# Kernel optimization log

Hardware: AMD Instinct MI355X
Metric: run time of the kernel (lower is better)

The kernel has to match this reference:

```python
import jax, jax.numpy as jnp
import numpy as np

WIN = 7
N = WIN * WIN  # 49 tokens per window
C = 384
H = 12
HD = C // H
B_ = 4096
NW = 64  # number of distinct window masks; must divide B_


def _relative_position_index(wh=WIN, ww=WIN):
    coords = np.stack(np.meshgrid(np.arange(wh), np.arange(ww), indexing='ij'))  # [2,wh,ww]
    cf = coords.reshape(2, -1)
    rel = cf[:, :, None] - cf[:, None, :]               # [2,N,N]
    rel = rel.transpose(1, 2, 0).astype(np.int32)       # [N,N,2]
    rel[:, :, 0] += wh - 1
    rel[:, :, 1] += ww - 1
    rel[:, :, 0] *= 2 * ww - 1
    return jnp.asarray(rel.sum(-1))                     # [N,N] int32


def setup_inputs() -> dict:
    key = jax.random.key(0)
    ks = jax.random.split(key, 8)
    std = 0.02
    return {
        'x': jax.random.normal(ks[0], (B_, N, C), jnp.float32),
        'mask': jnp.zeros((NW, N, N), jnp.float32),  # 0/-inf mask; zeros here
        'qkv_w': jax.random.normal(ks[1], (3 * C, C), jnp.float32) * std,
        'qkv_b': jnp.zeros((3 * C,), jnp.float32),
        'rpb_table': jax.random.normal(ks[2], ((2 * WIN - 1) ** 2, H), jnp.float32) * std,
        'proj_l_w': jax.random.normal(ks[3], (H, H), jnp.float32) * std,
        'proj_l_b': jnp.zeros((H,), jnp.float32),
        'proj_w_w': jax.random.normal(ks[4], (H, H), jnp.float32) * std,
        'proj_w_b': jnp.zeros((H,), jnp.float32),
        'proj_weight': jax.random.normal(ks[5], (C, C), jnp.float32) * std,
        'proj_bias': jnp.zeros((C,), jnp.float32),
        'rel_index': _relative_position_index(),
    }


def reference(x, mask, qkv_w, qkv_b, rpb_table, proj_l_w, proj_l_b,
              proj_w_w, proj_w_b, proj_weight, proj_bias, rel_index):
    B, n, c = x.shape
    scale = HD ** (-0.5)
    qkv = x @ qkv_w.T + qkv_b                     # [B,N,3C]
    q_out, k_out, v_out = jnp.split(qkv, 3, axis=-1)  # each [B,N,C]
    qkv5 = qkv.reshape(B, n, 3, H, HD)
    q = qkv5[:, :, 0].transpose(0, 2, 1, 3)       # [B,H,N,hd]
    k = qkv5[:, :, 1].transpose(0, 2, 1, 3)
    v = qkv5[:, :, 2].transpose(0, 2, 1, 3)
    attn = jnp.einsum('bhnd,bhmd->bhnm', q * scale, k)   # [B,H,N,N]
    bias = rpb_table[rel_index]                   # [N,N,H]
    attn = attn + bias.transpose(2, 0, 1)[None]
    # proj_l: linear mixing across heads (Linear acts on last dim after permute)
    attn = jnp.einsum('bhnm,gh->bgnm', attn, proj_l_w) + proj_l_b[None, :, None, None]
    nW = mask.shape[0]
    attn = attn.reshape(B // nW, nW, H, n, n) + mask[None, :, None]
    attn = attn.reshape(B, H, n, n)
    attn = jax.nn.softmax(attn, axis=-1)
    # proj_w: head mixing after softmax
    attn = jnp.einsum('bhnm,gh->bgnm', attn, proj_w_w) + proj_w_b[None, :, None, None]
    out = jnp.einsum('bhnm,bhmd->bnhd', attn, v).reshape(B, n, c)
    out = out @ proj_weight.T + proj_bias
    return (out, (q_out, k_out, v_out))
```

## Files before the change

### kernel.cpp

```cpp
#include <hip/hip_runtime.h>
#include <hip/hip_bf16.h>

#define TOK 49
#define NPT 2401
#define CDIM 384
#define NH 12
#define HDIM 32
#define NWIN 64
#define BTOT 4096
#define OUTSZ (BTOT * TOK * CDIM)
#define L2E 1.4426950408889634f

typedef __attribute__((ext_vector_type(8))) short bf16x8;
typedef __attribute__((ext_vector_type(4))) float f32x4;
typedef unsigned int uint32;
typedef unsigned short ushort_t;

__device__ inline ushort_t f2bf(float f) {
  uint32 u = __float_as_uint(f);
  u += 0x7FFF + ((u >> 16) & 1);
  return (ushort_t)(u >> 16);
}
__device__ inline uint32 pk2(float a, float b) {
  union { __hip_bfloat162 h; uint32 u; } x;
  x.h = __float22bfloat162_rn(float2{a, b});
  return x.u;
}
__device__ inline float bf2f(uint32 u) { return __uint_as_float((u & 0xffffu) << 16); }
__device__ inline bf16x8 pack8(float4 a, float4 b) {
  union { __hip_bfloat162 h[4]; bf16x8 v; } u;
  u.h[0] = __float22bfloat162_rn(float2{a.x, a.y});
  u.h[1] = __float22bfloat162_rn(float2{a.z, a.w});
  u.h[2] = __float22bfloat162_rn(float2{b.x, b.y});
  u.h[3] = __float22bfloat162_rn(float2{b.z, b.w});
  return u.v;
}
__device__ inline bf16x8 pack8f(const float* f) {
  union { __hip_bfloat162 h[4]; bf16x8 v; } u;
#pragma unroll
  for (int i = 0; i < 4; ++i) u.h[i] = __float22bfloat162_rn(float2{f[2*i], f[2*i+1]});
  return u.v;
}

__global__ void k_cvt(const float* __restrict__ src, ushort_t* __restrict__ dst, int n8) {
  int i = blockIdx.x * 256 + threadIdx.x;
  if (i >= n8) return;
  const float4* s = (const float4*)(src + (size_t)i * 8);
  float4 a = s[0], b = s[1];
  uint4 o;
  o.x = (uint32)f2bf(a.x) | ((uint32)f2bf(a.y) << 16);
  o.y = (uint32)f2bf(a.z) | ((uint32)f2bf(a.w) << 16);
  o.z = (uint32)f2bf(b.x) | ((uint32)f2bf(b.y) << 16);
  o.w = (uint32)f2bf(b.z) | ((uint32)f2bf(b.w) << 16);
  *(uint4*)(dst + (size_t)i * 8) = o;
}

__global__ void k_bias(const float* __restrict__ rpb, const float* __restrict__ plw,
                       const float* __restrict__ plb, float* __restrict__ bm) {
  int i = blockIdx.x * 256 + threadIdx.x;
  if (i >= 169 * 16) return;
  int rid = i >> 4, g = i & 15;
  float s = 0.f;
  if (g < NH) {
    s = plb[g];
#pragma unroll
    for (int h = 0; h < NH; ++h) s = fmaf(plw[g * NH + h], rpb[rid * NH + h], s);
    s *= L2E;
  }
  bm[i] = s;
}

__launch_bounds__(256)
__global__ void k_qkv_mfma(const ushort_t* __restrict__ Xb, const ushort_t* __restrict__ Wb,
                           const float* __restrict__ Bq, float* __restrict__ qslab) {
  __shared__ ushort_t As[128 * 32];
  __shared__ ushort_t Bs[128 * 32];
  const int bid = blockIdx.x;
  const int sw = (bid & 7) * 1764 + (bid >> 3);
  const int bx = sw / 9;
  const int by = sw - bx * 9;
  const int tid = threadIdx.x;
  const int l = tid & 63;
  const int wv = tid >> 6;
  const int wr = wv >> 1, wc = wv & 1;
  const int row0 = bx * 128;
  const int col0 = by * 128;

  f32x4 acc[4][4];
#pragma unroll
  for (int i = 0; i < 4; ++i)
#pragma unroll
    for (int j = 0; j < 4; ++j)
#pragma unroll
      for (int e = 0; e < 4; ++e) acc[i][j][e] = 0.f;

  for (int kb = 0; kb < CDIM; kb += 32) {
#pragma unroll
    for (int i = 0; i < 2; ++i) {
      int cid = tid + i * 256;
      int r = cid >> 2, c = cid & 3;
      uint4 v = *(const uint4*)&Xb[(size_t)(row0 + r) * CDIM + kb + c * 8];
      *(uint4*)&As[r * 32 + c * 8] = v;
      uint4 w = *(const uint4*)&Wb[(size_t)(col0 + r) * CDIM + kb + c * 8];
      *(uint4*)&Bs[r * 32 + c * 8] = w;
    }
    __syncthreads();
    bf16x8 af[4], bfr[4];
#pragma unroll
    for (int mt = 0; mt < 4; ++mt)
      af[mt] = *(const bf16x8*)&As[(wr * 64 + mt * 16 + (l & 15)) * 32 + (l >> 4) * 8];
#pragma unroll
    for (int nt = 0; nt < 4; ++nt)
      bfr[nt] = *(const bf16x8*)&Bs[(wc * 64 + nt * 16 + (l & 15)) * 32 + (l >> 4) * 8];
#pragma unroll
    for (int mt = 0; mt < 4; ++mt)
#pragma unroll
      for (int nt = 0; nt < 4; ++nt)
        acc[mt][nt] = __builtin_amdgcn_mfma_f32_16x16x32_bf16(af[mt], bfr[nt], acc[mt][nt], 0, 0, 0);
    __syncthreads();
  }

  const int slab = by / 3;
  const int cslab0 = col0 - slab * CDIM;
  float* dst = qslab + (size_t)slab * OUTSZ;
#pragma unroll
  for (int nt = 0; nt < 4; ++nt) {
    int colg = col0 + wc * 64 + nt * 16 + (l & 15);
    int colo = cslab0 + wc * 64 + nt * 16 + (l & 15);
    float bv = Bq[colg];
#pragma unroll
    for (int mt = 0; mt < 4; ++mt) {
      int rbase = row0 + wr * 64 + mt * 16 + (l >> 4) * 4;
#pragma unroll
      for (int j = 0; j < 4; ++j)
        dst[(size_t)(rbase + j) * CDIM + colo] = acc[mt][nt][j] + bv;
    }
  }
}

__launch_bounds__(1024, 8)
__global__ void k_attn9(const float* __restrict__ qslab, const float* __restrict__ kslab,
                        const float* __restrict__ vslab, const float* __restrict__ mask,
                        const float* __restrict__ bmg, const int* __restrict__ relidx,
                        const float* __restrict__ plw, const float* __restrict__ pww,
                        const float* __restrict__ pwb, float* __restrict__ xout) {
  __shared__ __align__(16) ushort_t SA[19976];
  __shared__ __align__(16) ushort_t PP[12 * 1400 + 416];
  __shared__ __align__(16) ushort_t bm16[169 * 12 + 4];
  __shared__ ushort_t ridx_s[1240];

  const int tid = threadIdx.x;
  const int b  = blockIdx.x >> 1;
  const int bh = blockIdx.x & 1;
  const int n0 = bh * 25;
  const int NR = bh ? 24 : 25;
  const size_t base = (size_t)b * TOK * CDIM;
  const int l = tid & 63, l15 = l & 15, l16 = l >> 4;
  const int wv = tid >> 6;
  const float SCL = 0.17677669529663687f * L2E;

  for (int i = tid; i < 169 * 12; i += 1024) {
    int rid = i / 12, g = i - rid * 12;
    bm16[i] = f2bf(bmg[rid * 16 + g]);
  }
  for (int i = tid; i < 1240; i += 1024) {
    int pg = i + n0 * 49; if (pg > 2400) pg = 2400;
    ridx_s[i] = (ushort_t)relidx[pg];
  }
  for (int p = tid; p < 1240; p += 1024) *(uint2*)&SA[p * 16 + 12] = uint2{0u, 0u};
  if (tid < 580) *(uint32*)&SA[18816 + tid * 2] = 0u;
  if (tid < 208) *(uint32*)&PP[12 * 1400 + tid * 2] = 0u;

  {
    const int art = wv >> 3;
    const int act = (wv >> 1) & 3;
    const int ah0 = (wv & 1) * 6;
    const int nrow = art * 16 + l15;
    const int mrow = act * 16 + l15;
    const bool qv = nrow < NR;
    const bool kv = mrow < TOK;
#pragma unroll
    for (int hp = 0; hp < 3; ++hp) {
      f32x4 s2[2];
#pragma unroll
      for (int hh = 0; hh < 2; ++hh) {
        int h = ah0 + hp * 2 + hh;
        bf16x8 af = {0,0,0,0,0,0,0,0}, bf = {0,0,0,0,0,0,0,0};
        if (qv) {
          const float4* qp = (const float4*)(qslab + base + (size_t)(n0 + nrow) * CDIM + h * HDIM + l16 * 8);
          af = pack8(qp[0], qp[1]);
        }
        if (kv) {
          const float4* kp = (const float4*)(kslab + base + (size_t)mrow * CDIM + h * HDIM + l16 * 8);
          bf = pack8(kp[0], kp[1]);
        }
        f32x4 z = {0.f, 0.f, 0.f, 0.f};
        s2[hh] = __builtin_amdgcn_mfma_f32_16x16x32_bf16(af, bf, z, 0, 0, 0);
      }
#pragma unroll
      for (int j = 0; j < 4; ++j) {
        int nj = art * 16 + l16 * 4 + j;
        if (nj < NR && kv)
          *(uint32*)&SA[(nj * 49 + mrow) * 16 + ah0 + hp * 2] = pk2(s2[0][j], s2[1][j]);
      }
    }
  }
  __syncthreads();

  {
    const float* maskw = mask + (size_t)(b & (NWIN - 1)) * NPT;
    float apf[8], bpf[8];
#pragma unroll
    for (int j = 0; j < 8; ++j) {
      int kj = l16 * 8 + j;
      apf[j] = (l15 < NH && kj < NH) ? plw[l15 * NH + kj] * SCL : 0.f;
      bpf[j] = (l15 < NH && kj < NH) ? pww[l15 * NH + kj] : 0.f;
    }
    const bf16x8 aplw = pack8f(apf);
    const bf16x8 bpww = pack8f(bpf);
    const float pwbv = (l15 < NH) ? pwb[l15] : 0.f;

    for (int nl = wv; nl < NR; nl += 16) {
      const int pb0 = nl * 49;
      float ev[4][4];
      float rs[4] = {0.f, 0.f, 0.f, 0.f};
#pragma unroll
      for (int mc = 0; mc < 4; ++mc) {
        int m = mc * 16 + l15;
        int pl = pb0 + m;
        bf16x8 sf = {0,0,0,0,0,0,0,0};
        if (l16 < 2) sf = *(const bf16x8*)&SA[pl * 16 + l16 * 8];
        int rid = (int)ridx_s[pl];
        uint2 bmu = *(const uint2*)&bm16[rid * 12 + l16 * 4];
        int pg = pl + n0 * 49; if (pg > 2400) pg = 2400;
        float mk = maskw[pg] * L2E;
        f32x4 cini = {bf2f(bmu.x) + mk, bf2f(bmu.x >> 16) + mk,
                      bf2f(bmu.y) + mk, bf2f(bmu.y >> 16) + mk};
        f32x4 o = __builtin_amdgcn_mfma_f32_16x16x32_bf16(aplw, sf, cini, 0, 0, 0);
        bool okm = (m < TOK);
#pragma unroll
        for (int j = 0; j < 4; ++j) {
          int g = l16 * 4 + j;
          float e = (okm && g < NH) ? exp2f(o[j]) : 0.f;
          ev[mc][j] = e;
          rs[j] += e;
        }
      }
#pragma unroll
      for (int d = 1; d < 16; d <<= 1)
#pragma unroll
        for (int j = 0; j < 4; ++j) rs[j] += __shfl_xor(rs[j], d, 64);
      float inv[4];
#pragma unroll
      for (int j = 0; j < 4; ++j) inv[j] = (rs[j] > 0.f) ? 1.f / rs[j] : 0.f;

#pragma unroll
      for (int mc = 0; mc < 4; ++mc) {
        int m = mc * 16 + l15;
        if (m < TOK) {
          uint2 w;
          w.x = pk2(ev[mc][0] * inv[0], ev[mc][1] * inv[1]);
          w.y = pk2(ev[mc][2] * inv[2], ev[mc][3] * inv[3]);
          *(uint2*)&SA[(pb0 + m) * 16 + l16 * 4] = w;
        }
      }
#pragma unroll
      for (int mc = 0; mc < 4; ++mc) {
        bf16x8 pf8 = {0,0,0,0,0,0,0,0};
        if (l16 < 2) pf8 = *(const bf16x8*)&SA[(pb0 + mc * 16 + l15) * 16 + l16 * 8];
        f32x4 cd = {pwbv, pwbv, pwbv, pwbv};
        f32x4 o = __builtin_amdgcn_mfma_f32_16x16x32_bf16(pf8, bpww, cd, 0, 0, 0);
        int m0 = mc * 16 + l16 * 4;
        if (l15 < NH && m0 < 56) {
          float z0 = (m0     < TOK) ? o[0] : 0.f;
          float z1 = (m0 + 1 < TOK) ? o[1] : 0.f;
          float z2 = (m0 + 2 < TOK) ? o[2] : 0.f;
          float z3 = (m0 + 3 < TOK) ? o[3] : 0.f;
          uint2 w;
          w.x = pk2(z0, z1);
          w.y = pk2(z2, z3);
          *(uint2*)&PP[l15 * 1400 + nl * 56 + m0] = w;
        }
      }
    }
  }
  __syncthreads();

  {
    ushort_t* Vt = SA;
    for (int i = tid; i < CDIM * 13; i += 1024) {
      int mq = i / CDIM, c = i - mq * CDIM;
      int m = mq * 4;
      float f0 = (m     < TOK) ? vslab[base + (size_t)(m    ) * CDIM + c] : 0.f;
      float f1 = (m + 1 < TOK) ? vslab[base + (size_t)(m + 1) * CDIM + c] : 0.f;
      float f2 = (m + 2 < TOK) ? vslab[base + (size_t)(m + 2) * CDIM + c] : 0.f;
      float f3 = (m + 3 < TOK) ? vslab[base + (size_t)(m + 3) * CDIM + c] : 0.f;
      uint2 u;
      u.x = pk2(f0, f1);
      u.y = pk2(f2, f3);
      *(uint2*)&Vt[c * 52 + mq * 4] = u;
    }
  }
  __syncthreads();

  {
    const ushort_t* Vt = SA;
    const int ert = wv >> 3;
    const int edt = (wv >> 2) & 1;
    const int egq = wv & 3;
#pragma unroll
    for (int gi = 0; gi < 3; ++gi) {
      int g = egq * 3 + gi;
      int col = g * HDIM + edt * 16 + l15;
      f32x4 acc = {0.f, 0.f, 0.f, 0.f};
#pragma unroll
      for (int ks = 0; ks < 2; ++ks) {
        bf16x8 pa8 = {0,0,0,0,0,0,0,0};
        bf16x8 vb8 = {0,0,0,0,0,0,0,0};
        if (!(ks == 1 && l16 == 3)) {
          pa8 = *(const bf16x8*)&PP[g * 1400 + (ert * 16 + l15) * 56 + ks * 32 + l16 * 8];
          uint2 lo = *(const uint2*)&Vt[col * 52 + ks * 32 + l16 * 8];
          uint2 hi = *(const uint2*)&Vt[col * 52 + ks * 32 + l16 * 8 + 4];
          union { uint32 u[4]; bf16x8 v; } uv;
          uv.u[0] = lo.x; uv.u[1] = lo.y; uv.u[2] = hi.x; uv.u[3] = hi.y;
          vb8 = uv.v;
        }
        acc = __builtin_amdgcn_mfma_f32_16x16x32_bf16(pa8, vb8, acc, 0, 0, 0);
      }
#pragma unroll
      for (int j = 0; j < 4; ++j) {
        int nlo = ert * 16 + l16 * 4 + j;
        if (nlo < NR)
          xout[base + (size_t)(n0 + nlo) * CDIM + col] = acc[j];
      }
    }
  }
}

__launch_bounds__(512, 4)
__global__ void k_proj3(float* __restrict__ Y, const float* __restrict__ W,
                        const float* __restrict__ Bv) {
  __shared__ __align__(16) ushort_t Asb[64 * 392];
  __shared__ __align__(16) ushort_t Bsb[384 * 40];
  const int tid = threadIdx.x;
  const int l = tid & 63, l15 = l & 15, l16 = l >> 4;
  const int wv = tid >> 6;
  const int wr = wv >> 2;
  const int wc = wv & 3;
  const int row0 = blockIdx.x * 64;

#pragma unroll
  for (int i = 0; i < 6; ++i) {
    int cid = tid + i * 512;
    int r = cid / 48, c8 = cid - (cid / 48) * 48;
    const float4* s = (const float4*)&Y[(size_t)(row0 + r) * CDIM + c8 * 8];
    float4 a = s[0], b = s[1];
    uint4 o;
    o.x = pk2(a.x, a.y); o.y = pk2(a.z, a.w);
    o.z = pk2(b.x, b.y); o.w = pk2(b.z, b.w);
    *(uint4*)&Asb[r * 392 + c8 * 8] = o;
  }

  f32x4 acc[2][6];
#pragma unroll
  for (int i = 0; i < 2; ++i)
#pragma unroll
    for (int j = 0; j < 6; ++j)
#pragma unroll
      for (int e = 0; e < 4; ++e) acc[i][j][e] = 0.f;

  for (int kb = 0; kb < 12; ++kb) {
    __syncthreads();
#pragma unroll
    for (int i = 0; i < 3; ++i) {
      int cid = tid + i * 512;
      int col = cid >> 2, k8 = cid & 3;
      const float4* s = (const float4*)&W[(size_t)col * CDIM + kb * 32 + k8 * 8];
      float4 a = s[0], b = s[1];
      uint4 o;
      o.x = pk2(a.x, a.y); o.y = pk2(a.z, a.w);
      o.z = pk2(b.x, b.y); o.w = pk2(b.z, b.w);
      *(uint4*)&Bsb[col * 40 + k8 * 8] = o;
    }
    __syncthreads();
    bf16x8 af[2], bfr[6];
#pragma unroll
    for (int mt = 0; mt < 2; ++mt)
      af[mt] = *(const bf16x8*)&Asb[(wr * 32 + mt * 16 + l15) * 392 + kb * 32 + l16 * 8];
#pragma unroll
    for (int nt = 0; nt < 6; ++nt)
      bfr[nt] = *(const bf16x8*)&Bsb[(wc * 96 + nt * 16 + l15) * 40 + l16 * 8];
#pragma unroll
    for (int mt = 0; mt < 2; ++mt)
#pragma unroll
      for (int nt = 0; nt < 6; ++nt)
        acc[mt][nt] = __builtin_amdgcn_mfma_f32_16x16x32_bf16(af[mt], bfr[nt], acc[mt][nt], 0, 0, 0);
  }

#pragma unroll
  for (int nt = 0; nt < 6; ++nt) {
    int col = wc * 96 + nt * 16 + l15;
    float bv = Bv[col];
#pragma unroll
    for (int mt = 0; mt < 2; ++mt) {
      int rbase = row0 + wr * 32 + mt * 16 + l16 * 4;
#pragma unroll
      for (int j = 0; j < 4; ++j)
        Y[(size_t)(rbase + j) * CDIM + col] = acc[mt][nt][j] + bv;
    }
  }
}

extern "C" void kernel_launch(void* const* d_in, const int* in_sizes, int n_in,
                              void* d_out, int out_size, void* d_ws, size_t ws_size,
                              hipStream_t stream) {
  const float* x      = (const float*)d_in[0];
  const float* mask   = (const float*)d_in[1];
  const float* qkv_w  = (const float*)d_in[2];
  const float* qkv_b  = (const float*)d_in[3];
  const float* rpb    = (const float*)d_in[4];
  const float* plw    = (const float*)d_in[5];
  const float* plb    = (const float*)d_in[6];
  const float* pww    = (const float*)d_in[7];
  const float* pwb    = (const float*)d_in[8];
  const float* projw  = (const float*)d_in[9];
  const float* projb  = (const float*)d_in[10];
  const int*   relidx = (const int*)d_in[11];

  float* out   = (float*)d_out;
  float* qslab = out + (size_t)OUTSZ;
  float* kslab = out + 2 * (size_t)OUTSZ;
  float* vslab = out + 3 * (size_t)OUTSZ;

  ushort_t* Xb = (ushort_t*)out;
  ushort_t* Wb = (ushort_t*)(out + 70000000);
  float*    bm = (float*)d_ws;

  k_cvt<<<(OUTSZ / 8 + 255) / 256, 256, 0, stream>>>(x, Xb, OUTSZ / 8);
  k_cvt<<<(3 * CDIM * CDIM / 8 + 255) / 256, 256, 0, stream>>>(qkv_w, Wb, 3 * CDIM * CDIM / 8);
  k_bias<<<(169 * 16 + 255) / 256, 256, 0, stream>>>(rpb, plw, plb, bm);

  k_qkv_mfma<<<(BTOT * TOK / 128) * 9, 256, 0, stream>>>(Xb, Wb, qkv_b, qslab);

  k_attn9<<<BTOT * 2, 1024, 0, stream>>>(qslab, kslab, vslab, mask, bm, relidx,
                                         plw, pww, pwb, out);

  k_proj3<<<BTOT * TOK / 64, 512, 0, stream>>>(out, projw, projb);
}
```

Before: 1.350 ms.

## Fuse output projection into attention kernel via LDS-staged bf16 attention output

The output projection GEMM now runs at the end of the attention kernel, which previously ran as a separate kernel. Each block stages its per-window attention output as bf16 in shared memory. Its 16 waves then multiply that tile against a pre-converted bf16 projection weight read from global memory, adding the bias before the store. This removes the fp32 round trip of the attention output through HBM and one kernel launch. In exchange, every block re-reads the 384x384 weight from L2/global with no LDS reuse, the MFMA work is uneven across waves (only 8 of 16 take a second column tile), and the 25/24-row halves are padded to 32 rows.

```diff
diff --git a/kernel.cpp b/kernel.cpp
--- a/kernel.cpp
+++ b/kernel.cpp
@@ -139,11 +139,12 @@
 }
 
 __launch_bounds__(1024, 8)
-__global__ void k_attn9(const float* __restrict__ qslab, const float* __restrict__ kslab,
-                        const float* __restrict__ vslab, const float* __restrict__ mask,
-                        const float* __restrict__ bmg, const int* __restrict__ relidx,
-                        const float* __restrict__ plw, const float* __restrict__ pww,
-                        const float* __restrict__ pwb, float* __restrict__ xout) {
+__global__ void k_attn10(const float* __restrict__ qslab, const float* __restrict__ kslab,
+                         const float* __restrict__ vslab, const float* __restrict__ mask,
+                         const float* __restrict__ bmg, const int* __restrict__ relidx,
+                         const float* __restrict__ plw, const float* __restrict__ pww,
+                         const float* __restrict__ pwb, const ushort_t* __restrict__ Wb2,
+                         const float* __restrict__ pjb, float* __restrict__ xout) {
   __shared__ __align__(16) ushort_t SA[19976];
   __shared__ __align__(16) ushort_t PP[12 * 1400 + 416];
   __shared__ __align__(16) ushort_t bm16[169 * 12 + 4];
@@ -303,11 +304,12 @@
   }
   __syncthreads();
 
+  f32x4 acc3[3];
+  const int ert = wv >> 3;
+  const int edt = (wv >> 2) & 1;
+  const int egq = wv & 3;
   {
     const ushort_t* Vt = SA;
-    const int ert = wv >> 3;
-    const int edt = (wv >> 2) & 1;
-    const int egq = wv & 3;
 #pragma unroll
     for (int gi = 0; gi < 3; ++gi) {
       int g = egq * 3 + gi;
@@ -327,86 +329,78 @@
         }
         acc = __builtin_amdgcn_mfma_f32_16x16x32_bf16(pa8, vb8, acc, 0, 0, 0);
       }
+      acc3[gi] = acc;
+    }
+  }
+  __syncthreads();
+
+  {
+    ushort_t* AO = SA;
+#pragma unroll
+    for (int gi = 0; gi < 3; ++gi) {
+      int g = egq * 3 + gi;
+      int col = g * HDIM + edt * 16 + l15;
 #pragma unroll
       for (int j = 0; j < 4; ++j) {
         int nlo = ert * 16 + l16 * 4 + j;
-        if (nlo < NR)
-          xout[base + (size_t)(n0 + nlo) * CDIM + col] = acc[j];
-      }
-    }
-  }
-}
-
-__launch_bounds__(512, 4)
-__global__ void k_proj3(float* __restrict__ Y, const float* __restrict__ W,
-                        const float* __restrict__ Bv) {
-  __shared__ __align__(16) ushort_t Asb[64 * 392];
-  __shared__ __align__(16) ushort_t Bsb[384 * 40];
-  const int tid = threadIdx.x;
-  const int l = tid & 63, l15 = l & 15, l16 = l >> 4;
-  const int wv = tid >> 6;
-  const int wr = wv >> 2;
-  const int wc = wv & 3;
-  const int row0 = blockIdx.x * 64;
-
-#pragma unroll
-  for (int i = 0; i < 6; ++i) {
-    int cid = tid + i * 512;
-    int r = cid / 48, c8 = cid - (cid / 48) * 48;
-    const float4* s = (const float4*)&Y[(size_t)(row0 + r) * CDIM + c8 * 8];
-    float4 a = s[0], b = s[1];
-    uint4 o;
-    o.x = pk2(a.x, a.y); o.y = pk2(a.z, a.w);
-    o.z = pk2(b.x, b.y); o.w = pk2(b.z, b.w);
-    *(uint4*)&Asb[r * 392 + c8 * 8] = o;
-  }
-
-  f32x4 acc[2][6];
-#pragma unroll
-  for (int i = 0; i < 2; ++i)
-#pragma unroll
-    for (int j = 0; j < 6; ++j)
-#pragma unroll
-      for (int e = 0; e < 4; ++e) acc[i][j][e] = 0.f;
-
-  for (int kb = 0; kb < 12; ++kb) {
-    __syncthreads();
-#pragma unroll
-    for (int i = 0; i < 3; ++i) {
-      int cid = tid + i * 512;
-      int col = cid >> 2, k8 = cid & 3;
-      const float4* s = (const float4*)&W[(size_t)col * CDIM + kb * 32 + k8 * 8];
-      float4 a = s[0], b = s[1];
-      uint4 o;
-      o.x = pk2(a.x, a.y); o.y = pk2(a.z, a.w);
-      o.z = pk2(b.x, b.y); o.w = pk2(b.z, b.w);
-      *(uint4*)&Bsb[col * 40 + k8 * 8] = o;
-    }
-    __syncthreads();
-    bf16x8 af[2], bfr[6];
-#pragma unroll
-    for (int mt = 0; mt < 2; ++mt)
-      af[mt] = *(const bf16x8*)&Asb[(wr * 32 + mt * 16 + l15) * 392 + kb * 32 + l16 * 8];
-#pragma unroll
-    for (int nt = 0; nt < 6; ++nt)
-      bfr[nt] = *(const bf16x8*)&Bsb[(wc * 96 + nt * 16 + l15) * 40 + l16 * 8];
-#pragma unroll
-    for (int mt = 0; mt < 2; ++mt)
-#pragma unroll
-      for (int nt = 0; nt < 6; ++nt)
-        acc[mt][nt] = __builtin_amdgcn_mfma_f32_16x16x32_bf16(af[mt], bfr[nt], acc[mt][nt], 0, 0, 0);
-  }
-
-#pragma unroll
-  for (int nt = 0; nt < 6; ++nt) {
-    int col = wc * 96 + nt * 16 + l15;
-    float bv = Bv[col];
-#pragma unroll
-    for (int mt = 0; mt < 2; ++mt) {
-      int rbase = row0 + wr * 32 + mt * 16 + l16 * 4;
-#pragma unroll
-      for (int j = 0; j < 4; ++j)
-        Y[(size_t)(rbase + j) * CDIM + col] = acc[mt][nt][j] + bv;
+        AO[nlo * 392 + col] = f2bf(acc3[gi][j]);
+      }
+    }
+  }
+  __syncthreads();
+
+  {
+    const ushort_t* AO = SA;
+    f32x4 pacc[2][2];
+#pragma unroll
+    for (int r = 0; r < 2; ++r)
+#pragma unroll
+      for (int c = 0; c < 2; ++c)
+#pragma unroll
+        for (int e = 0; e < 4; ++e) pacc[r][c][e] = 0.f;
+
+    const bool two = (wv < 8);
+    for (int ks = 0; ks < 12; ++ks) {
+      bf16x8 af0 = *(const bf16x8*)&AO[(l15     ) * 392 + ks * 32 + l16 * 8];
+      bf16x8 af1 = *(const bf16x8*)&AO[(16 + l15) * 392 + ks * 32 + l16 * 8];
+      {
+        int ct = wv;
+        uint4 wq = *(const uint4*)&Wb2[(size_t)(ct * 16 + l15) * CDIM + ks * 32 + l16 * 8];
+        union { uint4 u; bf16x8 v; } uw; uw.u = wq;
+        pacc[0][0] = __builtin_amdgcn_mfma_f32_16x16x32_bf16(af0, uw.v, pacc[0][0], 0, 0, 0);
+        pacc[1][0] = __builtin_amdgcn_mfma_f32_16x16x32_bf16(af1, uw.v, pacc[1][0], 0, 0, 0);
+      }
+      if (two) {
+        int ct = wv + 16;
+        uint4 wq = *(const uint4*)&Wb2[(size_t)(ct * 16 + l15) * CDIM + ks * 32 + l16 * 8];
+        union { uint4 u; bf16x8 v; } uw; uw.u = wq;
+        pacc[0][1] = __builtin_amdgcn_mfma_f32_16x16x32_bf16(af0, uw.v, pacc[0][1], 0, 0, 0);
+        pacc[1][1] = __builtin_amdgcn_mfma_f32_16x16x32_bf16(af1, uw.v, pacc[1][1], 0, 0, 0);
+      }
+    }
+    {
+      int col = wv * 16 + l15;
+      float pb = pjb[col];
+#pragma unroll
+      for (int rt2 = 0; rt2 < 2; ++rt2)
+#pragma unroll
+        for (int j = 0; j < 4; ++j) {
+          int row = rt2 * 16 + l16 * 4 + j;
+          if (row < NR)
+            xout[base + (size_t)(n0 + row) * CDIM + col] = pacc[rt2][0][j] + pb;
+        }
+    }
+    if (two) {
+      int col = (wv + 16) * 16 + l15;
+      float pb = pjb[col];
+#pragma unroll
+      for (int rt2 = 0; rt2 < 2; ++rt2)
+#pragma unroll
+        for (int j = 0; j < 4; ++j) {
+          int row = rt2 * 16 + l16 * 4 + j;
+          if (row < NR)
+            xout[base + (size_t)(n0 + row) * CDIM + col] = pacc[rt2][1][j] + pb;
+        }
     }
   }
 }
@@ -432,18 +426,18 @@
   float* kslab = out + 2 * (size_t)OUTSZ;
   float* vslab = out + 3 * (size_t)OUTSZ;
 
-  ushort_t* Xb = (ushort_t*)out;
-  ushort_t* Wb = (ushort_t*)(out + 70000000);
-  float*    bm = (float*)d_ws;
+  ushort_t* Xb  = (ushort_t*)out;
+  ushort_t* Wb  = (ushort_t*)(out + 70000000);
+  float*    bm  = (float*)d_ws;
+  ushort_t* Wb2 = (ushort_t*)((float*)d_ws + 4096);
 
   k_cvt<<<(OUTSZ / 8 + 255) / 256, 256, 0, stream>>>(x, Xb, OUTSZ / 8);
   k_cvt<<<(3 * CDIM * CDIM / 8 + 255) / 256, 256, 0, stream>>>(qkv_w, Wb, 3 * CDIM * CDIM / 8);
+  k_cvt<<<(CDIM * CDIM / 8 + 255) / 256, 256, 0, stream>>>(projw, Wb2, CDIM * CDIM / 8);
   k_bias<<<(169 * 16 + 255) / 256, 256, 0, stream>>>(rpb, plw, plb, bm);
 
   k_qkv_mfma<<<(BTOT * TOK / 128) * 9, 256, 0, stream>>>(Xb, Wb, qkv_b, qslab);
 
-  k_attn9<<<BTOT * 2, 1024, 0, stream>>>(qslab, kslab, vslab, mask, bm, relidx,
-                                         plw, pww, pwb, out);
-
-  k_proj3<<<BTOT * TOK / 64, 512, 0, stream>>>(out, projw, projb);
-}
+  k_attn10<<<BTOT * 2, 1024, 0, stream>>>(qslab, kslab, vslab, mask, bm, relidx,
+                                          plw, pww, pwb, Wb2, projb, out);
+}
```

Result: no change. 1.362 ms (+0.9%).
